# Kernel tuning notes

Measured on AMD Instinct MI355X. Metric: run time of the kernel, lower is better.

Reference implementation:

```python
import jax, jax.numpy as jnp
import numpy as np

B, S, D, H = 2, 2048, 1024, 16
DK = D // H  # 64
THETA = 10000.0


def _rope_tables(max_seq_len, d_k, theta):
    dim_idx = jnp.arange(0, d_k // 2, dtype=jnp.float32)
    freqs = 1.0 / theta ** (2.0 * dim_idx / d_k)
    pos = jnp.arange(0, max_seq_len, dtype=jnp.float32)
    ang = jnp.outer(pos, freqs)  # [S, d_k//2]
    return jnp.sin(ang), jnp.cos(ang)


def setup_inputs() -> dict:
    key = jax.random.key(0)
    ks = jax.random.split(key, 5)
    scale = 0.02
    x = jax.random.normal(ks[0], (B, S, D), dtype=jnp.float32)
    w_q = jax.random.normal(ks[1], (D, D), dtype=jnp.float32) * scale
    w_k = jax.random.normal(ks[2], (D, D), dtype=jnp.float32) * scale
    w_v = jax.random.normal(ks[3], (D, D), dtype=jnp.float32) * scale
    w_o = jax.random.normal(ks[4], (D, D), dtype=jnp.float32) * scale
    sin_tab, cos_tab = _rope_tables(S, DK, THETA)
    token_positions = jnp.broadcast_to(jnp.arange(S, dtype=jnp.int32), (B, S))
    return {"x": x, "w_q": w_q, "w_k": w_k, "w_v": w_v, "w_o": w_o,
            "sin_tab": sin_tab, "cos_tab": cos_tab,
            "token_positions": token_positions}


def _apply_rope(t, sin, cos):
    # t: [B, H, S, DK]; sin/cos: [B, 1, S, DK//2]
    t_even = t[..., 0::2]
    t_odd = t[..., 1::2]
    r_even = cos * t_even - sin * t_odd
    r_odd = sin * t_even + cos * t_odd
    # re-interleave even/odd back into last dim
    out = jnp.stack([r_even, r_odd], axis=-1)  # [B,H,S,DK//2,2]
    return out.reshape(t.shape)


def reference(x, w_q, w_k, w_v, w_o, sin_tab, cos_tab, token_positions):
    b, s, d = x.shape
    q = (x @ w_q.T).reshape(b, s, H, DK).transpose(0, 2, 1, 3)  # [B,H,S,DK]
    k = (x @ w_k.T).reshape(b, s, H, DK).transpose(0, 2, 1, 3)
    v = (x @ w_v.T).reshape(b, s, H, DK).transpose(0, 2, 1, 3)

    sin = sin_tab[token_positions][:, None, :, :]  # [B,1,S,DK//2]
    cos = cos_tab[token_positions][:, None, :, :]
    q = _apply_rope(q, sin, cos)
    k = _apply_rope(k, sin, cos)

    scores = jnp.einsum('bhqd,bhkd->bhqk', q, k) / jnp.sqrt(jnp.float32(DK))
    causal = jnp.tril(jnp.ones((s, s), dtype=bool))  # keep lower triangle
    scores = jnp.where(causal, scores, -jnp.inf)
    probs = jax.nn.softmax(scores, axis=-1)
    attn = jnp.einsum('bhqk,bhkd->bhqd', probs, v)
    attn = attn.transpose(0, 2, 1, 3).reshape(b, s, d)
    return attn @ w_o.T
```

## Files before the change

kernel.cpp:

```cpp
#include <hip/hip_runtime.h>
#include <hip/hip_bf16.h>
#include <cstdint>

#define B_ 2
#define S_ 2048
#define D_ 1024
#define H_ 16
#define DK_ 64
#define HALF_ 32

typedef short bf16x8 __attribute__((ext_vector_type(8)));
typedef float f32x4  __attribute__((ext_vector_type(4)));
typedef unsigned int u32;

static __device__ __forceinline__ unsigned short bfbits(float f) {
    __hip_bfloat16 h = __float2bfloat16(f);
    unsigned short u; __builtin_memcpy(&u, &h, 2); return u;
}
static __device__ __forceinline__ unsigned pack2bf(float a, float b) {
    return (unsigned)bfbits(a) | ((unsigned)bfbits(b) << 16);
}

static __device__ __forceinline__ void gload_lds16(const void* g, void* l) {
    __builtin_amdgcn_global_load_lds(
        (const __attribute__((address_space(1))) u32*)(uintptr_t)g,
        (__attribute__((address_space(3))) u32*)(uintptr_t)l,
        16, 0, 0);
}

__global__ __launch_bounds__(256) void to_bf16_kernel(
    const float* __restrict__ x,
    const float* __restrict__ wq, const float* __restrict__ wk,
    const float* __restrict__ wv, const float* __restrict__ wo,
    const float* __restrict__ sin_tab, const float* __restrict__ cos_tab,
    __hip_bfloat16* __restrict__ xb,
    __hip_bfloat16* __restrict__ wqb, __hip_bfloat16* __restrict__ wkb,
    __hip_bfloat16* __restrict__ wvb, __hip_bfloat16* __restrict__ wob,
    float2* __restrict__ sctab)
{
    const int seg = blockIdx.y;
    if (seg == 8) {
        if (blockIdx.x >= 64) return;
        size_t i = ((size_t)blockIdx.x * 256 + threadIdx.x) * 4;
        float4 c = *reinterpret_cast<const float4*>(cos_tab + i);
        float4 s = *reinterpret_cast<const float4*>(sin_tab + i);
        float4* dst = reinterpret_cast<float4*>(sctab + i);
        dst[0] = make_float4(c.x, s.x, c.y, s.y);
        dst[1] = make_float4(c.z, s.z, c.w, s.w);
        return;
    }
    const float* src;
    __hip_bfloat16* dst;
    size_t off = 0;
    if (seg < 4)       { src = x;  dst = xb;  off = (size_t)seg << 20; }
    else if (seg == 4) { src = wq; dst = wqb; }
    else if (seg == 5) { src = wk; dst = wkb; }
    else if (seg == 6) { src = wv; dst = wvb; }
    else               { src = wo; dst = wob; }
    size_t i = off + ((size_t)blockIdx.x * 256 + threadIdx.x) * 4;
    float4 v = *reinterpret_cast<const float4*>(src + i);
    ushort4 u = make_ushort4(bfbits(v.x), bfbits(v.y), bfbits(v.z), bfbits(v.w));
    *reinterpret_cast<ushort4*>(dst + i) = u;
}

template<int MODE>
__global__ __launch_bounds__(256) void mfma_gemm_kernel(
    const __hip_bfloat16* __restrict__ A,
    const __hip_bfloat16* __restrict__ Wq, const __hip_bfloat16* __restrict__ Wk,
    const __hip_bfloat16* __restrict__ Wv,
    __hip_bfloat16* __restrict__ out_q, __hip_bfloat16* __restrict__ out_k,
    __hip_bfloat16* __restrict__ out_v,
    float* __restrict__ out_f32,
    const float2* __restrict__ sctab,
    const int* __restrict__ tpos)
{
    constexpr int K = 1024;
    const int which = (MODE == 0) ? blockIdx.z : 3;
    const __hip_bfloat16* __restrict__ W =
        (MODE == 1) ? Wq : (which == 0 ? Wq : which == 1 ? Wk : Wv);

    __shared__ __align__(16) unsigned char As[2][128 * 4 * 16];
    __shared__ __align__(16) unsigned char Bs[2][128 * 4 * 16];

    const int tid = threadIdx.x;
    const int wid = tid >> 6;
    const int l   = tid & 63;
    const int g   = l >> 4;
    const int i16 = l & 15;
    const int wr  = wid >> 1, wc = wid & 1;

    const int wg   = blockIdx.x;
    const int tile = (wg & 7) * 32 + (wg >> 3);
    const int row0 = (tile >> 3) * 128;
    const int col0 = (tile & 7) * 128;

    const __hip_bfloat16* Abase = A + (size_t)row0 * K;
    const __hip_bfloat16* Wbase = W + (size_t)col0 * K;

    f32x4 acc[4][4];
    const f32x4 zero = {0.f, 0.f, 0.f, 0.f};
    #pragma unroll
    for (int mi = 0; mi < 4; ++mi)
        #pragma unroll
        for (int ni = 0; ni < 4; ++ni) acc[mi][ni] = zero;

    int a_off[4], b_off[4];
    #pragma unroll
    for (int f = 0; f < 4; ++f) {
        int ra = wr * 64 + f * 16 + i16;
        a_off[f] = (ra * 4 + (g ^ ((ra >> 1) & 3))) * 16;
        int rb = wc * 64 + f * 16 + i16;
        b_off[f] = (rb * 4 + (g ^ ((rb >> 1) & 3))) * 16;
    }

    int st_goff[2], st_loff[2];
    #pragma unroll
    for (int it = 0; it < 2; ++it) {
        int c = it * 256 + wid * 64 + l;
        int row = c >> 2;
        int kc = (c & 3) ^ ((row >> 1) & 3);
        st_goff[it] = row * K + kc * 8;
        st_loff[it] = (it * 256 + wid * 64) * 16;
    }

    #pragma unroll
    for (int it = 0; it < 2; ++it) {
        gload_lds16(Abase + st_goff[it], &As[0][0] + st_loff[it]);
        gload_lds16(Wbase + st_goff[it], &Bs[0][0] + st_loff[it]);
    }
    __syncthreads();

    for (int t = 0; t < K / 32; ++t) {
        const int cur = t & 1;
        if (t + 1 < K / 32) {
            const int k1 = (t + 1) * 32;
            #pragma unroll
            for (int it = 0; it < 2; ++it) {
                gload_lds16(Abase + k1 + st_goff[it], &As[cur ^ 1][0] + st_loff[it]);
                gload_lds16(Wbase + k1 + st_goff[it], &Bs[cur ^ 1][0] + st_loff[it]);
            }
        }
        bf16x8 af[4], bfr[4];
        #pragma unroll
        for (int f = 0; f < 4; ++f) {
            af[f]  = *reinterpret_cast<const bf16x8*>(&As[cur][0] + a_off[f]);
            bfr[f] = *reinterpret_cast<const bf16x8*>(&Bs[cur][0] + b_off[f]);
        }
        #pragma unroll
        for (int mi = 0; mi < 4; ++mi)
            #pragma unroll
            for (int ni = 0; ni < 4; ++ni)
                acc[mi][ni] = __builtin_amdgcn_mfma_f32_16x16x32_bf16(
                    af[mi], bfr[ni], acc[mi][ni], 0, 0, 0);
        __syncthreads();
    }

    if (MODE == 0) {
        __hip_bfloat16* __restrict__ outp =
            which == 0 ? out_q : which == 1 ? out_k : out_v;
        const int head = (col0 >> 6) + wc;
        #pragma unroll
        for (int mi = 0; mi < 4; ++mi) {
            #pragma unroll
            for (int r = 0; r < 4; ++r) {
                const int gi = row0 + wr * 64 + mi * 16 + g * 4 + r;
                const int b_ = gi >> 11;
                const int s_ = gi & (S_ - 1);
                const int pos = tpos[gi];
                const float2* sc = sctab + pos * HALF_;
                __hip_bfloat16* orow =
                    outp + (((size_t)b_ * H_ + head) * S_ + s_) * DK_;
                #pragma unroll
                for (int ni = 0; ni < 4; ++ni) {
                    float val = acc[mi][ni][r];
                    float other = __shfl_xor(val, 1, 64);
                    const int dk = ni * 16 + i16;
                    float res;
                    if (which < 2) {
                        float2 cs = sc[ni * 8 + (i16 >> 1)];
                        res = (i16 & 1) ? fmaf(cs.y, other, cs.x * val)
                                        : (cs.x * val - cs.y * other);
                    } else {
                        res = val;
                    }
                    if (which == 0) res *= 0.180336880f;
                    orow[dk] = __float2bfloat16(res);
                }
            }
        }
    } else {
        #pragma unroll
        for (int mi = 0; mi < 4; ++mi) {
            #pragma unroll
            for (int r = 0; r < 4; ++r) {
                const int gi = row0 + wr * 64 + mi * 16 + g * 4 + r;
                float* orow = out_f32 + (size_t)gi * D_ + col0 + wc * 64;
                #pragma unroll
                for (int ni = 0; ni < 4; ++ni)
                    orow[ni * 16 + i16] = acc[mi][ni][r];
            }
        }
    }
}

__global__ __launch_bounds__(256) void flash_mfma_kernel(
    const __hip_bfloat16* __restrict__ q,
    const __hip_bfloat16* __restrict__ k,
    const __hip_bfloat16* __restrict__ v,
    __hip_bfloat16* __restrict__ attn)
{
    __shared__ __align__(16) unsigned char Ks[2][64 * 128];
    __shared__ __align__(16) unsigned char Vt[2][64 * 128];
    __shared__ __align__(16) unsigned char Ps[4][16 * 128];

    const int tid = threadIdx.x;
    const int w   = tid >> 6;
    const int l   = tid & 63;
    const int g   = l >> 4;
    const int i16 = l & 15;

    const int wgid = blockIdx.x;
    const int xcd  = wgid & 7;
    const int idx  = wgid >> 3;
    const int bh   = xcd * 4 + (idx & 3);
    const int qsb  = 31 - (idx >> 2);

    const size_t base = (size_t)bh * S_ * DK_;
    const __hip_bfloat16* kb_ = k + base;
    const __hip_bfloat16* vb_ = v + base;
    const int nt = qsb + 1;

    int ksrc[2], kdst[2];
    #pragma unroll
    for (int it = 0; it < 2; ++it) {
        int c = it * 256 + tid;
        int krow = c >> 3;
        int kchunk = (c & 7) ^ (krow & 7);
        ksrc[it] = krow * DK_ + kchunk * 8;
        kdst[it] = c * 16;
    }
    const int vd8_0 = w;
    const int vd8_1 = 4 + w;
    unsigned char* const pw = &Ps[w][0];

    const int qrow = qsb * 64 + w * 16 + i16;

    bf16x8 qf0, qf1;
    {
        const __hip_bfloat16* qp = q + base + (size_t)qrow * DK_ + g * 8;
        qf0 = *reinterpret_cast<const bf16x8*>(qp);
        qf1 = *reinterpret_cast<const bf16x8*>(qp + 32);
    }

    f32x4 o[4] = {};
    float m_run = -1e30f, l_run = 0.0f;

    #pragma unroll
    for (int it = 0; it < 2; ++it)
        gload_lds16(kb_ + ksrc[it], &Ks[0][0] + kdst[it]);
    {
        float4 vv0 = *reinterpret_cast<const float4*>(vb_ + l * DK_ + vd8_0 * 8);
        float4 vv1 = *reinterpret_cast<const float4*>(vb_ + l * DK_ + vd8_1 * 8);
        const unsigned short* u0 = reinterpret_cast<const unsigned short*>(&vv0);
        const unsigned short* u1 = reinterpret_cast<const unsigned short*>(&vv1);
        #pragma unroll
        for (int s = 0; s < 8; ++s) {
            int d0 = vd8_0 * 8 + s;
            *reinterpret_cast<unsigned short*>(&Vt[0][0] + d0 * 128 +
                (((l >> 3) ^ (d0 & 7)) << 4) + (l & 7) * 2) = u0[s];
            int d1 = vd8_1 * 8 + s;
            *reinterpret_cast<unsigned short*>(&Vt[0][0] + d1 * 128 +
                (((l >> 3) ^ (d1 & 7)) << 4) + (l & 7) * 2) = u1[s];
        }
    }
    __syncthreads();

    for (int t = 0; t < nt; ++t) {
        const int cur = t & 1;
        const bool pre = (t + 1 < nt);
        float4 vv0, vv1;
        if (pre) {
            const size_t toff = (size_t)(t + 1) * 64 * DK_;
            #pragma unroll
            for (int it = 0; it < 2; ++it)
                gload_lds16(kb_ + toff + ksrc[it], &Ks[cur ^ 1][0] + kdst[it]);
            vv0 = *reinterpret_cast<const float4*>(vb_ + toff + l * DK_ + vd8_0 * 8);
            vv1 = *reinterpret_cast<const float4*>(vb_ + toff + l * DK_ + vd8_1 * 8);
        }

        f32x4 s_acc[4] = {};
        __builtin_amdgcn_s_setprio(1);
        #pragma unroll
        for (int jf = 0; jf < 4; ++jf) {
            int row = jf * 16 + i16;
            bf16x8 ak0 = *reinterpret_cast<const bf16x8*>(
                &Ks[cur][0] + row * 128 + ((g ^ (row & 7)) << 4));
            s_acc[jf] = __builtin_amdgcn_mfma_f32_16x16x32_bf16(
                ak0, qf0, s_acc[jf], 0, 0, 0);
            bf16x8 ak1 = *reinterpret_cast<const bf16x8*>(
                &Ks[cur][0] + row * 128 + (((4 + g) ^ (row & 7)) << 4));
            s_acc[jf] = __builtin_amdgcn_mfma_f32_16x16x32_bf16(
                ak1, qf1, s_acc[jf], 0, 0, 0);
        }
        __builtin_amdgcn_s_setprio(0);

        if (t == nt - 1) {
            #pragma unroll
            for (int jf = 0; jf < 4; ++jf)
                #pragma unroll
                for (int r = 0; r < 4; ++r)
                    if (t * 64 + jf * 16 + g * 4 + r > qrow)
                        s_acc[jf][r] = -1e30f;
        }

        float mx0 = fmaxf(fmaxf(s_acc[0][0], s_acc[0][1]),
                          fmaxf(s_acc[0][2], s_acc[0][3]));
        float mx1 = fmaxf(fmaxf(s_acc[1][0], s_acc[1][1]),
                          fmaxf(s_acc[1][2], s_acc[1][3]));
        float mx2 = fmaxf(fmaxf(s_acc[2][0], s_acc[2][1]),
                          fmaxf(s_acc[2][2], s_acc[2][3]));
        float mx3 = fmaxf(fmaxf(s_acc[3][0], s_acc[3][1]),
                          fmaxf(s_acc[3][2], s_acc[3][3]));
        float vmax = fmaxf(fmaxf(mx0, mx1), fmaxf(mx2, mx3));
        vmax = fmaxf(vmax, __shfl_xor(vmax, 16, 64));
        vmax = fmaxf(vmax, __shfl_xor(vmax, 32, 64));

        if (!__all(vmax <= m_run + 11.5f)) {
            float m_new = fmaxf(m_run, vmax);
            float factor = __builtin_amdgcn_exp2f(m_run - m_new);
            m_run = m_new;
            l_run *= factor;
            #pragma unroll
            for (int df = 0; df < 4; ++df)
                #pragma unroll
                for (int r = 0; r < 4; ++r)
                    o[df][r] *= factor;
        }

        float p[4][4];
        float psum = 0.0f;
        #pragma unroll
        for (int jf = 0; jf < 4; ++jf)
            #pragma unroll
            for (int r = 0; r < 4; ++r) {
                p[jf][r] = __builtin_amdgcn_exp2f(s_acc[jf][r] - m_run);
                psum += p[jf][r];
            }
        psum += __shfl_xor(psum, 16, 64);
        psum += __shfl_xor(psum, 32, 64);
        l_run += psum;

        #pragma unroll
        for (int jf = 0; jf < 4; ++jf)
            #pragma unroll
            for (int r0 = 0; r0 < 4; r0 += 2) {
                unsigned pk = pack2bf(p[jf][r0], p[jf][r0 + 1]);
                int jj = jf * 16 + g * 4 + r0;
                *reinterpret_cast<unsigned*>(pw + i16 * 128 +
                    ((jj * 2) ^ ((i16 & 7) << 4))) = pk;
            }

        __builtin_amdgcn_s_setprio(1);
        #pragma unroll
        for (int jc = 0; jc < 2; ++jc) {
            bf16x8 bp = *reinterpret_cast<const bf16x8*>(pw + i16 * 128 +
                (((jc * 4 + g) ^ (i16 & 7)) << 4));
            #pragma unroll
            for (int df = 0; df < 4; ++df) {
                int row = df * 16 + i16;
                bf16x8 av = *reinterpret_cast<const bf16x8*>(
                    &Vt[cur][0] + row * 128 +
                    (((jc * 4 + g) ^ (row & 7)) << 4));
                o[df] = __builtin_amdgcn_mfma_f32_16x16x32_bf16(
                    av, bp, o[df], 0, 0, 0);
            }
        }
        __builtin_amdgcn_s_setprio(0);

        if (pre) {
            unsigned char* vtb = &Vt[cur ^ 1][0];
            const unsigned short* u0 = reinterpret_cast<const unsigned short*>(&vv0);
            const unsigned short* u1 = reinterpret_cast<const unsigned short*>(&vv1);
            #pragma unroll
            for (int s = 0; s < 8; ++s) {
                int d0 = vd8_0 * 8 + s;
                *reinterpret_cast<unsigned short*>(vtb + d0 * 128 +
                    (((l >> 3) ^ (d0 & 7)) << 4) + (l & 7) * 2) = u0[s];
                int d1 = vd8_1 * 8 + s;
                *reinterpret_cast<unsigned short*>(vtb + d1 * 128 +
                    (((l >> 3) ^ (d1 & 7)) << 4) + (l & 7) * 2) = u1[s];
            }
        }
        __syncthreads();
    }

    const float inv_l = 1.0f / l_run;
    const int b_ = bh >> 4, h_ = bh & 15;
    __hip_bfloat16* orow = attn + ((size_t)b_ * S_ + qrow) * D_ + h_ * 64;
    #pragma unroll
    for (int df = 0; df < 4; ++df) {
        ushort4 uo = make_ushort4(
            bfbits(o[df][0] * inv_l), bfbits(o[df][1] * inv_l),
            bfbits(o[df][2] * inv_l), bfbits(o[df][3] * inv_l));
        *reinterpret_cast<ushort4*>(orow + df * 16 + g * 4) = uo;
    }
}

extern "C" void kernel_launch(void* const* d_in, const int* in_sizes, int n_in,
                              void* d_out, int out_size, void* d_ws, size_t ws_size,
                              hipStream_t stream) {
    const float* x       = (const float*)d_in[0];
    const float* w_q     = (const float*)d_in[1];
    const float* w_k     = (const float*)d_in[2];
    const float* w_v     = (const float*)d_in[3];
    const float* w_o     = (const float*)d_in[4];
    const float* sin_tab = (const float*)d_in[5];
    const float* cos_tab = (const float*)d_in[6];
    const int*   tpos    = (const int*)d_in[7];
    float* out = (float*)d_out;

    const size_t nM  = (size_t)B_ * S_ * D_;
    const size_t nW  = (size_t)D_ * D_;
    __hip_bfloat16* xb   = (__hip_bfloat16*)d_ws;
    __hip_bfloat16* wqb  = xb  + nM;
    __hip_bfloat16* wkb  = wqb + nW;
    __hip_bfloat16* wvb  = wkb + nW;
    __hip_bfloat16* wob  = wvb + nW;
    __hip_bfloat16* q_ws = wob + nW;
    __hip_bfloat16* k_ws = q_ws + nM;
    __hip_bfloat16* v_ws = k_ws + nM;
    __hip_bfloat16* a_ws = v_ws + nM;
    float2*         sct  = (float2*)(a_ws + nM);

    to_bf16_kernel<<<dim3(1024, 9), 256, 0, stream>>>(
        x, w_q, w_k, w_v, w_o, sin_tab, cos_tab,
        xb, wqb, wkb, wvb, wob, sct);
    mfma_gemm_kernel<0><<<dim3(256, 1, 3), 256, 0, stream>>>(
        xb, wqb, wkb, wvb, q_ws, k_ws, v_ws, nullptr, sct, tpos);
    flash_mfma_kernel<<<1024, 256, 0, stream>>>(
        q_ws, k_ws, v_ws, a_ws);
    mfma_gemm_kernel<1><<<dim3(256, 1, 1), 256, 0, stream>>>(
        a_ws, wob, nullptr, nullptr, nullptr, nullptr, nullptr, out,
        sct, tpos);
}
```

Measured before the change: 135.4 us.

## Process 128 query rows per flash-attention block, two 16-row tiles per wave

Each workgroup in the flash attention kernel now covers 128 query rows, with every wave holding two 16-row Q tiles. Each K/V tile staged in LDS is therefore reused across twice as many query rows, and the grid is halved to 512 blocks. Per-tile activity flags skip the softmax and PV work for causally masked halves, and launch bounds now request two blocks per CU. The cost is more registers per thread (two sets of accumulators and softmax state), fewer blocks to balance the causal load, and more divergent control flow.

```diff
diff --git a/kernel.cpp b/kernel.cpp
--- a/kernel.cpp
+++ b/kernel.cpp
@@ -203,7 +203,7 @@
     }
 }
 
-__global__ __launch_bounds__(256) void flash_mfma_kernel(
+__global__ __launch_bounds__(256, 2) void flash_mfma_kernel(
     const __hip_bfloat16* __restrict__ q,
     const __hip_bfloat16* __restrict__ k,
     const __hip_bfloat16* __restrict__ v,
@@ -211,7 +211,7 @@
 {
     __shared__ __align__(16) unsigned char Ks[2][64 * 128];
     __shared__ __align__(16) unsigned char Vt[2][64 * 128];
-    __shared__ __align__(16) unsigned char Ps[4][16 * 128];
+    __shared__ __align__(16) unsigned char Ps[4][2][16 * 128];
 
     const int tid = threadIdx.x;
     const int w   = tid >> 6;
@@ -223,12 +223,12 @@
     const int xcd  = wgid & 7;
     const int idx  = wgid >> 3;
     const int bh   = xcd * 4 + (idx & 3);
-    const int qsb  = 31 - (idx >> 2);
+    const int qsb  = 15 - (idx >> 2);
 
     const size_t base = (size_t)bh * S_ * DK_;
     const __hip_bfloat16* kb_ = k + base;
     const __hip_bfloat16* vb_ = v + base;
-    const int nt = qsb + 1;
+    const int nt = 2 * qsb + 2;
 
     int ksrc[2], kdst[2];
     #pragma unroll
@@ -241,19 +241,24 @@
     }
     const int vd8_0 = w;
     const int vd8_1 = 4 + w;
-    unsigned char* const pw = &Ps[w][0];
-
-    const int qrow = qsb * 64 + w * 16 + i16;
-
-    bf16x8 qf0, qf1;
+    unsigned char* const pw0 = &Ps[w][0][0];
+    unsigned char* const pw1 = &Ps[w][1][0];
+
+    const int qrow0 = qsb * 128 + w * 32 + i16;
+    const int qrow1 = qrow0 + 16;
+
+    bf16x8 qf00, qf01, qf10, qf11;
     {
-        const __hip_bfloat16* qp = q + base + (size_t)qrow * DK_ + g * 8;
-        qf0 = *reinterpret_cast<const bf16x8*>(qp);
-        qf1 = *reinterpret_cast<const bf16x8*>(qp + 32);
-    }
-
-    f32x4 o[4] = {};
-    float m_run = -1e30f, l_run = 0.0f;
+        const __hip_bfloat16* qp0 = q + base + (size_t)qrow0 * DK_ + g * 8;
+        qf00 = *reinterpret_cast<const bf16x8*>(qp0);
+        qf01 = *reinterpret_cast<const bf16x8*>(qp0 + 32);
+        const __hip_bfloat16* qp1 = q + base + (size_t)qrow1 * DK_ + g * 8;
+        qf10 = *reinterpret_cast<const bf16x8*>(qp1);
+        qf11 = *reinterpret_cast<const bf16x8*>(qp1 + 32);
+    }
+
+    f32x4 o0[4] = {}, o1[4] = {};
+    float m0 = -1e30f, l0 = 0.0f, m1 = -1e30f, l1 = 0.0f;
 
     #pragma unroll
     for (int it = 0; it < 2; ++it)
@@ -288,91 +293,138 @@
             vv1 = *reinterpret_cast<const float4*>(vb_ + toff + l * DK_ + vd8_1 * 8);
         }
 
-        f32x4 s_acc[4] = {};
+        const int wbase = qsb * 128 + w * 32;
+        const bool act0 = (t * 64 <= wbase + 15);
+        const bool act1 = (t * 64 <= wbase + 31);
+
+        f32x4 s0[4] = {}, s1[4] = {};
         __builtin_amdgcn_s_setprio(1);
         #pragma unroll
         for (int jf = 0; jf < 4; ++jf) {
             int row = jf * 16 + i16;
             bf16x8 ak0 = *reinterpret_cast<const bf16x8*>(
                 &Ks[cur][0] + row * 128 + ((g ^ (row & 7)) << 4));
-            s_acc[jf] = __builtin_amdgcn_mfma_f32_16x16x32_bf16(
-                ak0, qf0, s_acc[jf], 0, 0, 0);
             bf16x8 ak1 = *reinterpret_cast<const bf16x8*>(
                 &Ks[cur][0] + row * 128 + (((4 + g) ^ (row & 7)) << 4));
-            s_acc[jf] = __builtin_amdgcn_mfma_f32_16x16x32_bf16(
-                ak1, qf1, s_acc[jf], 0, 0, 0);
+            s0[jf] = __builtin_amdgcn_mfma_f32_16x16x32_bf16(ak0, qf00, s0[jf], 0, 0, 0);
+            s1[jf] = __builtin_amdgcn_mfma_f32_16x16x32_bf16(ak0, qf10, s1[jf], 0, 0, 0);
+            s0[jf] = __builtin_amdgcn_mfma_f32_16x16x32_bf16(ak1, qf01, s0[jf], 0, 0, 0);
+            s1[jf] = __builtin_amdgcn_mfma_f32_16x16x32_bf16(ak1, qf11, s1[jf], 0, 0, 0);
         }
         __builtin_amdgcn_s_setprio(0);
 
-        if (t == nt - 1) {
+        if (t * 64 + 63 > wbase) {
             #pragma unroll
             for (int jf = 0; jf < 4; ++jf)
                 #pragma unroll
-                for (int r = 0; r < 4; ++r)
-                    if (t * 64 + jf * 16 + g * 4 + r > qrow)
-                        s_acc[jf][r] = -1e30f;
-        }
-
-        float mx0 = fmaxf(fmaxf(s_acc[0][0], s_acc[0][1]),
-                          fmaxf(s_acc[0][2], s_acc[0][3]));
-        float mx1 = fmaxf(fmaxf(s_acc[1][0], s_acc[1][1]),
-                          fmaxf(s_acc[1][2], s_acc[1][3]));
-        float mx2 = fmaxf(fmaxf(s_acc[2][0], s_acc[2][1]),
-                          fmaxf(s_acc[2][2], s_acc[2][3]));
-        float mx3 = fmaxf(fmaxf(s_acc[3][0], s_acc[3][1]),
-                          fmaxf(s_acc[3][2], s_acc[3][3]));
-        float vmax = fmaxf(fmaxf(mx0, mx1), fmaxf(mx2, mx3));
-        vmax = fmaxf(vmax, __shfl_xor(vmax, 16, 64));
-        vmax = fmaxf(vmax, __shfl_xor(vmax, 32, 64));
-
-        if (!__all(vmax <= m_run + 11.5f)) {
-            float m_new = fmaxf(m_run, vmax);
-            float factor = __builtin_amdgcn_exp2f(m_run - m_new);
-            m_run = m_new;
-            l_run *= factor;
-            #pragma unroll
-            for (int df = 0; df < 4; ++df)
-                #pragma unroll
-                for (int r = 0; r < 4; ++r)
-                    o[df][r] *= factor;
-        }
-
-        float p[4][4];
-        float psum = 0.0f;
-        #pragma unroll
-        for (int jf = 0; jf < 4; ++jf)
-            #pragma unroll
-            for (int r = 0; r < 4; ++r) {
-                p[jf][r] = __builtin_amdgcn_exp2f(s_acc[jf][r] - m_run);
-                psum += p[jf][r];
-            }
-        psum += __shfl_xor(psum, 16, 64);
-        psum += __shfl_xor(psum, 32, 64);
-        l_run += psum;
-
-        #pragma unroll
-        for (int jf = 0; jf < 4; ++jf)
-            #pragma unroll
-            for (int r0 = 0; r0 < 4; r0 += 2) {
-                unsigned pk = pack2bf(p[jf][r0], p[jf][r0 + 1]);
-                int jj = jf * 16 + g * 4 + r0;
-                *reinterpret_cast<unsigned*>(pw + i16 * 128 +
-                    ((jj * 2) ^ ((i16 & 7) << 4))) = pk;
-            }
+                for (int r = 0; r < 4; ++r) {
+                    int kcol = t * 64 + jf * 16 + g * 4 + r;
+                    if (kcol > qrow0) s0[jf][r] = -1e30f;
+                    if (kcol > qrow1) s1[jf][r] = -1e30f;
+                }
+        }
+
+        float va0 = fmaxf(fmaxf(fmaxf(s0[0][0], s0[0][1]), fmaxf(s0[0][2], s0[0][3])),
+                          fmaxf(fmaxf(s0[1][0], s0[1][1]), fmaxf(s0[1][2], s0[1][3])));
+        float vb0 = fmaxf(fmaxf(fmaxf(s0[2][0], s0[2][1]), fmaxf(s0[2][2], s0[2][3])),
+                          fmaxf(fmaxf(s0[3][0], s0[3][1]), fmaxf(s0[3][2], s0[3][3])));
+        float vmax0 = fmaxf(va0, vb0);
+        float va1 = fmaxf(fmaxf(fmaxf(s1[0][0], s1[0][1]), fmaxf(s1[0][2], s1[0][3])),
+                          fmaxf(fmaxf(s1[1][0], s1[1][1]), fmaxf(s1[1][2], s1[1][3])));
+        float vb1 = fmaxf(fmaxf(fmaxf(s1[2][0], s1[2][1]), fmaxf(s1[2][2], s1[2][3])),
+                          fmaxf(fmaxf(s1[3][0], s1[3][1]), fmaxf(s1[3][2], s1[3][3])));
+        float vmax1 = fmaxf(va1, vb1);
+        vmax0 = fmaxf(vmax0, __shfl_xor(vmax0, 16, 64));
+        vmax0 = fmaxf(vmax0, __shfl_xor(vmax0, 32, 64));
+        vmax1 = fmaxf(vmax1, __shfl_xor(vmax1, 16, 64));
+        vmax1 = fmaxf(vmax1, __shfl_xor(vmax1, 32, 64));
+
+        bool ok = true;
+        if (act0) ok = ok && (vmax0 <= m0 + 11.5f);
+        if (act1) ok = ok && (vmax1 <= m1 + 11.5f);
+        if (!__all(ok)) {
+            if (act0) {
+                float mn = fmaxf(m0, vmax0);
+                float f = __builtin_amdgcn_exp2f(m0 - mn);
+                m0 = mn; l0 *= f;
+                #pragma unroll
+                for (int df = 0; df < 4; ++df)
+                    #pragma unroll
+                    for (int r = 0; r < 4; ++r) o0[df][r] *= f;
+            }
+            if (act1) {
+                float mn = fmaxf(m1, vmax1);
+                float f = __builtin_amdgcn_exp2f(m1 - mn);
+                m1 = mn; l1 *= f;
+                #pragma unroll
+                for (int df = 0; df < 4; ++df)
+                    #pragma unroll
+                    for (int r = 0; r < 4; ++r) o1[df][r] *= f;
+            }
+        }
+
+        if (act0) {
+            float p[4][4], psum = 0.0f;
+            #pragma unroll
+            for (int jf = 0; jf < 4; ++jf)
+                #pragma unroll
+                for (int r = 0; r < 4; ++r) {
+                    p[jf][r] = __builtin_amdgcn_exp2f(s0[jf][r] - m0);
+                    psum += p[jf][r];
+                }
+            psum += __shfl_xor(psum, 16, 64);
+            psum += __shfl_xor(psum, 32, 64);
+            l0 += psum;
+            #pragma unroll
+            for (int jf = 0; jf < 4; ++jf)
+                #pragma unroll
+                for (int r0 = 0; r0 < 4; r0 += 2) {
+                    unsigned pk = pack2bf(p[jf][r0], p[jf][r0 + 1]);
+                    int jj = jf * 16 + g * 4 + r0;
+                    *reinterpret_cast<unsigned*>(pw0 + i16 * 128 +
+                        ((jj * 2) ^ ((i16 & 7) << 4))) = pk;
+                }
+        }
+        if (act1) {
+            float p[4][4], psum = 0.0f;
+            #pragma unroll
+            for (int jf = 0; jf < 4; ++jf)
+                #pragma unroll
+                for (int r = 0; r < 4; ++r) {
+                    p[jf][r] = __builtin_amdgcn_exp2f(s1[jf][r] - m1);
+                    psum += p[jf][r];
+                }
+            psum += __shfl_xor(psum, 16, 64);
+            psum += __shfl_xor(psum, 32, 64);
+            l1 += psum;
+            #pragma unroll
+            for (int jf = 0; jf < 4; ++jf)
+                #pragma unroll
+                for (int r0 = 0; r0 < 4; r0 += 2) {
+                    unsigned pk = pack2bf(p[jf][r0], p[jf][r0 + 1]);
+                    int jj = jf * 16 + g * 4 + r0;
+                    *reinterpret_cast<unsigned*>(pw1 + i16 * 128 +
+                        ((jj * 2) ^ ((i16 & 7) << 4))) = pk;
+                }
+        }
 
         __builtin_amdgcn_s_setprio(1);
         #pragma unroll
         for (int jc = 0; jc < 2; ++jc) {
-            bf16x8 bp = *reinterpret_cast<const bf16x8*>(pw + i16 * 128 +
-                (((jc * 4 + g) ^ (i16 & 7)) << 4));
+            bf16x8 bp0, bp1;
+            if (act0) bp0 = *reinterpret_cast<const bf16x8*>(pw0 + i16 * 128 +
+                          (((jc * 4 + g) ^ (i16 & 7)) << 4));
+            if (act1) bp1 = *reinterpret_cast<const bf16x8*>(pw1 + i16 * 128 +
+                          (((jc * 4 + g) ^ (i16 & 7)) << 4));
             #pragma unroll
             for (int df = 0; df < 4; ++df) {
                 int row = df * 16 + i16;
                 bf16x8 av = *reinterpret_cast<const bf16x8*>(
-                    &Vt[cur][0] + row * 128 +
-                    (((jc * 4 + g) ^ (row & 7)) << 4));
-                o[df] = __builtin_amdgcn_mfma_f32_16x16x32_bf16(
-                    av, bp, o[df], 0, 0, 0);
+                    &Vt[cur][0] + row * 128 + (((jc * 4 + g) ^ (row & 7)) << 4));
+                if (act0) o0[df] = __builtin_amdgcn_mfma_f32_16x16x32_bf16(
+                              av, bp0, o0[df], 0, 0, 0);
+                if (act1) o1[df] = __builtin_amdgcn_mfma_f32_16x16x32_bf16(
+                              av, bp1, o1[df], 0, 0, 0);
             }
         }
         __builtin_amdgcn_s_setprio(0);
@@ -394,15 +446,28 @@
         __syncthreads();
     }
 
-    const float inv_l = 1.0f / l_run;
     const int b_ = bh >> 4, h_ = bh & 15;
-    __hip_bfloat16* orow = attn + ((size_t)b_ * S_ + qrow) * D_ + h_ * 64;
-    #pragma unroll
-    for (int df = 0; df < 4; ++df) {
-        ushort4 uo = make_ushort4(
-            bfbits(o[df][0] * inv_l), bfbits(o[df][1] * inv_l),
-            bfbits(o[df][2] * inv_l), bfbits(o[df][3] * inv_l));
-        *reinterpret_cast<ushort4*>(orow + df * 16 + g * 4) = uo;
+    {
+        const float inv_l = 1.0f / l0;
+        __hip_bfloat16* orow = attn + ((size_t)b_ * S_ + qrow0) * D_ + h_ * 64;
+        #pragma unroll
+        for (int df = 0; df < 4; ++df) {
+            ushort4 uo = make_ushort4(
+                bfbits(o0[df][0] * inv_l), bfbits(o0[df][1] * inv_l),
+                bfbits(o0[df][2] * inv_l), bfbits(o0[df][3] * inv_l));
+            *reinterpret_cast<ushort4*>(orow + df * 16 + g * 4) = uo;
+        }
+    }
+    {
+        const float inv_l = 1.0f / l1;
+        __hip_bfloat16* orow = attn + ((size_t)b_ * S_ + qrow1) * D_ + h_ * 64;
+        #pragma unroll
+        for (int df = 0; df < 4; ++df) {
+            ushort4 uo = make_ushort4(
+                bfbits(o1[df][0] * inv_l), bfbits(o1[df][1] * inv_l),
+                bfbits(o1[df][2] * inv_l), bfbits(o1[df][3] * inv_l));
+            *reinterpret_cast<ushort4*>(orow + df * 16 + g * 4) = uo;
+        }
     }
 }
 
@@ -437,7 +502,7 @@
         xb, wqb, wkb, wvb, wob, sct);
     mfma_gemm_kernel<0><<<dim3(256, 1, 3), 256, 0, stream>>>(
         xb, wqb, wkb, wvb, q_ws, k_ws, v_ws, nullptr, sct, tpos);
-    flash_mfma_kernel<<<1024, 256, 0, stream>>>(
+    flash_mfma_kernel<<<512, 256, 0, stream>>>(
         q_ws, k_ws, v_ws, a_ws);
     mfma_gemm_kernel<1><<<dim3(256, 1, 1), 256, 0, stream>>>(
         a_ws, wob, nullptr, nullptr, nullptr, nullptr, nullptr, out,
```

New measurement: 160.7 us. 18.8% more time.
